# Kernel optimization log

Hardware: AMD Instinct MI355X
Metric: run time of the kernel (lower is better)

## Reference

```python
import jax, jax.numpy as jnp
import numpy as np

G = 500          # num graphs
NODES_PER_G = 1000
EDGES_PER_G = 2000
N = G * NODES_PER_G   # 500_000 total nodes
E = G * EDGES_PER_G   # 1_000_000 total edges
DN, DE, DG, DO = 128, 64, 128, 128


def setup_inputs() -> dict:
    key = jax.random.key(0)
    ks = jax.random.split(key, 7)
    return {
        "node_features": jax.random.normal(ks[0], (N, DN), dtype=jnp.float32),
        "edge_features": jax.random.normal(ks[1], (E, DE), dtype=jnp.float32),
        "global_features": jax.random.normal(ks[2], (G, DG), dtype=jnp.float32),
        "W_node": jax.random.normal(ks[3], (DO, DN), dtype=jnp.float32) / np.sqrt(DN),
        "W_edges": jax.random.normal(ks[4], (DO, DE), dtype=jnp.float32) / np.sqrt(DE),
        "W_global": jax.random.normal(ks[5], (DO, DG), dtype=jnp.float32) / np.sqrt(DG),
        "bias": jax.random.normal(ks[6], (DO,), dtype=jnp.float32) * 0.01,
        "num_nodes_by_graph": jnp.full((G,), NODES_PER_G, dtype=jnp.int32),
        "num_edges_by_graph": jnp.full((G,), EDGES_PER_G, dtype=jnp.int32),
    }


def _segment_mean(feats, lengths, num_segments, total):
    # segment ids from per-graph lengths (segment_lengths_to_ids)
    ids = jnp.repeat(jnp.arange(num_segments, dtype=jnp.int32), lengths,
                     total_repeat_length=total)
    s = jax.ops.segment_sum(feats, ids, num_segments=num_segments)
    cnt = jnp.maximum(lengths, 1).astype(feats.dtype)[:, None]
    return s / cnt


def reference(node_features, edge_features, global_features,
              W_node, W_edges, W_global, bias,
              num_nodes_by_graph, num_edges_by_graph):
    # mean-aggregate nodes/edges per graph, then linear projections summed
    node_agg = _segment_mean(node_features, num_nodes_by_graph, G, N)   # [G, DN]
    edge_agg = _segment_mean(edge_features, num_edges_by_graph, G, E)   # [G, DE]
    out = (jnp.einsum('gd,od->go', node_agg, W_node)
           + jnp.einsum('gd,od->go', edge_agg, W_edges)
           + jnp.einsum('gd,od->go', global_features, W_global)
           + bias)
    return out
```

## Files before the change

kernel.cpp:

```cpp
#include <hip/hip_runtime.h>


#define DN 128
#define DE 64
#define DO 128
#define NODE_SPLIT 4
#define EDGE_SPLIT 8

typedef float f4v __attribute__((ext_vector_type(4)));

__device__ __forceinline__ f4v nt_load(const f4v* p) {
    return __builtin_nontemporal_load(p);
}

__global__ __launch_bounds__(512) void scan_offsets_kernel(
    const int* __restrict__ nlen, const int* __restrict__ elen, int G,
    int* __restrict__ noff, int* __restrict__ eoff)
{
    __shared__ int sn[512], se[512];
    __shared__ int carry_n, carry_e;
    const int t = threadIdx.x;
    if (t == 0) { carry_n = 0; carry_e = 0; }
    __syncthreads();

    for (int base = 0; base < G; base += 512) {
        const int idx = base + t;
        const int vn = (idx < G) ? nlen[idx] : 0;
        const int ve = (idx < G) ? elen[idx] : 0;
        sn[t] = vn; se[t] = ve;
        __syncthreads();
        for (int off = 1; off < 512; off <<= 1) {
            const int an = (t >= off) ? sn[t - off] : 0;
            const int ae = (t >= off) ? se[t - off] : 0;
            __syncthreads();
            sn[t] += an; se[t] += ae;
            __syncthreads();
        }
        if (idx < G) {
            noff[idx] = carry_n + sn[t] - vn;
            eoff[idx] = carry_e + se[t] - ve;
        }
        __syncthreads();
        if (t == 0) {
            const int last = (G - base < 512) ? (G - base - 1) : 511;
            carry_n += sn[last];
            carry_e += se[last];
        }
        __syncthreads();
    }
}

__global__ __launch_bounds__(256) void agg_kernel(
    const float* __restrict__ nodes, const float* __restrict__ edges,
    const int* __restrict__ noff, const int* __restrict__ eoff,
    const int* __restrict__ nlen, const int* __restrict__ elen,
    float* __restrict__ nsum, float* __restrict__ esum, int G)
{
    __shared__ f4v sm[256];
    const int b = blockIdx.x;
    const int t = threadIdx.x;

    if (b < G * NODE_SPLIT) {
        const int g = b / NODE_SPLIT;
        const int c = b % NODE_SPLIT;
        const int len = nlen[g];
        const int off = noff[g];
        const int chunk = (len + NODE_SPLIT - 1) / NODE_SPLIT;
        const int r0 = c * chunk;
        const int r1 = (r0 + chunk < len) ? (r0 + chunk) : len;
        const int span = (r1 > r0) ? (r1 - r0) : 0;
        const int main_end = r0 + (span & ~31);

        const int col = t & 31;
        const int rl  = t >> 5;
        const f4v* __restrict__ base = (const f4v*)nodes;

        f4v a0 = {0.f,0.f,0.f,0.f}, a1 = a0, a2 = a0, a3 = a0;
        for (int rr = r0 + rl * 4; rr < main_end; rr += 32) {
            const size_t p = (size_t)(off + rr) * (DN / 4) + col;
            a0 += nt_load(base + p);
            a1 += nt_load(base + p + (DN / 4));
            a2 += nt_load(base + p + 2 * (DN / 4));
            a3 += nt_load(base + p + 3 * (DN / 4));
        }
        for (int r = main_end + rl; r < r1; r += 8) {
            a0 += nt_load(base + (size_t)(off + r) * (DN / 4) + col);
        }
        const f4v acc = (a0 + a1) + (a2 + a3);

        sm[t] = acc;
        __syncthreads();
        for (int s = 128; s >= 32; s >>= 1) {
            if (t < s) sm[t] += sm[t + s];
            __syncthreads();
        }
        if (t < 32) {
            const f4v v = sm[t];
            float* dst = &nsum[(size_t)g * DN + col * 4];
            atomicAdd(dst + 0, v.x);
            atomicAdd(dst + 1, v.y);
            atomicAdd(dst + 2, v.z);
            atomicAdd(dst + 3, v.w);
        }
    } else {
        const int bb = b - G * NODE_SPLIT;
        const int g = bb / EDGE_SPLIT;
        const int c = bb % EDGE_SPLIT;
        const int len = elen[g];
        const int off = eoff[g];
        const int chunk = (len + EDGE_SPLIT - 1) / EDGE_SPLIT;
        const int r0 = c * chunk;
        const int r1 = (r0 + chunk < len) ? (r0 + chunk) : len;
        const int span = (r1 > r0) ? (r1 - r0) : 0;
        const int main_end = r0 + (span & ~63);

        const int col = t & 15;
        const int rl  = t >> 4;
        const f4v* __restrict__ base = (const f4v*)edges;

        f4v a0 = {0.f,0.f,0.f,0.f}, a1 = a0, a2 = a0, a3 = a0;
        for (int rr = r0 + rl * 4; rr < main_end; rr += 64) {
            const size_t p = (size_t)(off + rr) * (DE / 4) + col;
            a0 += nt_load(base + p);
            a1 += nt_load(base + p + (DE / 4));
            a2 += nt_load(base + p + 2 * (DE / 4));
            a3 += nt_load(base + p + 3 * (DE / 4));
        }
        for (int r = main_end + rl; r < r1; r += 16) {
            a0 += nt_load(base + (size_t)(off + r) * (DE / 4) + col);
        }
        const f4v acc = (a0 + a1) + (a2 + a3);

        sm[t] = acc;
        __syncthreads();
        for (int s = 128; s >= 16; s >>= 1) {
            if (t < s) sm[t] += sm[t + s];
            __syncthreads();
        }
        if (t < 16) {
            const f4v v = sm[t];
            float* dst = &esum[(size_t)g * DE + col * 4];
            atomicAdd(dst + 0, v.x);
            atomicAdd(dst + 1, v.y);
            atomicAdd(dst + 2, v.z);
            atomicAdd(dst + 3, v.w);
        }
    }
}

__global__ __launch_bounds__(128) void finalize_kernel(
    const float* __restrict__ nsum, const float* __restrict__ esum,
    const float* __restrict__ glob,
    const float* __restrict__ Wn, const float* __restrict__ We,
    const float* __restrict__ Wg, const float* __restrict__ bias,
    const int* __restrict__ nlen, const int* __restrict__ elen,
    float* __restrict__ out)
{
    __shared__ float sn[DN], se_[DE], sg[DN];
    const int g = blockIdx.x;
    const int o = threadIdx.x;

    const int nl = nlen[g];
    const int el = elen[g];
    const float inv_n = 1.0f / (float)((nl > 1) ? nl : 1);
    const float inv_e = 1.0f / (float)((el > 1) ? el : 1);

    sn[o] = nsum[(size_t)g * DN + o] * inv_n;
    sg[o] = glob[(size_t)g * DN + o];
    if (o < DE) se_[o] = esum[(size_t)g * DE + o] * inv_e;
    __syncthreads();

    float acc = bias[o];
    const float4* __restrict__ wn = (const float4*)(Wn + (size_t)o * DN);
    const float4* __restrict__ wg = (const float4*)(Wg + (size_t)o * DN);
    const float4* __restrict__ we = (const float4*)(We + (size_t)o * DE);
    const float4* s4n = (const float4*)sn;
    const float4* s4g = (const float4*)sg;
    const float4* s4e = (const float4*)se_;

    #pragma unroll
    for (int i = 0; i < DN / 4; ++i) {
        const float4 a = wn[i], v = s4n[i];
        acc += a.x * v.x + a.y * v.y + a.z * v.z + a.w * v.w;
    }
    #pragma unroll
    for (int i = 0; i < DN / 4; ++i) {
        const float4 a = wg[i], v = s4g[i];
        acc += a.x * v.x + a.y * v.y + a.z * v.z + a.w * v.w;
    }
    #pragma unroll
    for (int i = 0; i < DE / 4; ++i) {
        const float4 a = we[i], v = s4e[i];
        acc += a.x * v.x + a.y * v.y + a.z * v.z + a.w * v.w;
    }
    out[(size_t)g * DO + o] = acc;
}

extern "C" void kernel_launch(void* const* d_in, const int* in_sizes, int n_in,
                              void* d_out, int out_size, void* d_ws, size_t ws_size,
                              hipStream_t stream)
{
    const float* nodes = (const float*)d_in[0];
    const float* edges = (const float*)d_in[1];
    const float* glob  = (const float*)d_in[2];
    const float* Wn    = (const float*)d_in[3];
    const float* We    = (const float*)d_in[4];
    const float* Wg    = (const float*)d_in[5];
    const float* bias  = (const float*)d_in[6];
    const int*   nlen  = (const int*)d_in[7];
    const int*   elen  = (const int*)d_in[8];
    float*       out   = (float*)d_out;

    const int G = in_sizes[7];

    float* nsum = (float*)d_ws;
    float* esum = nsum + (size_t)G * DN;
    int*   noff = (int*)(esum + (size_t)G * DE);
    int*   eoff = noff + G;

    hipMemsetAsync(d_ws, 0, (size_t)G * (DN + DE) * sizeof(float), stream);

    scan_offsets_kernel<<<1, 512, 0, stream>>>(nlen, elen, G, noff, eoff);

    const int agg_blocks = G * (NODE_SPLIT + EDGE_SPLIT);
    agg_kernel<<<agg_blocks, 256, 0, stream>>>(nodes, edges, noff, eoff,
                                               nlen, elen, nsum, esum, G);

    finalize_kernel<<<G, 128, 0, stream>>>(nsum, esum, glob, Wn, We, Wg, bias,
                                           nlen, elen, out);
}
```

Before: 481.2 us.

## Remove scan kernel and memset; compute offsets in-block and write partial sums

After: 475.1 us. No clear change (-1.3%).

```diff
diff --git a/kernel.cpp b/kernel.cpp
--- a/kernel.cpp
+++ b/kernel.cpp
@@ -5,7 +5,7 @@
 #define DE 64
 #define DO 128
 #define NODE_SPLIT 4
-#define EDGE_SPLIT 8
+#define EDGE_SPLIT 4
 
 typedef float f4v __attribute__((ext_vector_type(4)));
 
@@ -13,64 +13,41 @@
     return __builtin_nontemporal_load(p);
 }
 
-__global__ __launch_bounds__(512) void scan_offsets_kernel(
-    const int* __restrict__ nlen, const int* __restrict__ elen, int G,
-    int* __restrict__ noff, int* __restrict__ eoff)
-{
-    __shared__ int sn[512], se[512];
-    __shared__ int carry_n, carry_e;
-    const int t = threadIdx.x;
-    if (t == 0) { carry_n = 0; carry_e = 0; }
-    __syncthreads();
-
-    for (int base = 0; base < G; base += 512) {
-        const int idx = base + t;
-        const int vn = (idx < G) ? nlen[idx] : 0;
-        const int ve = (idx < G) ? elen[idx] : 0;
-        sn[t] = vn; se[t] = ve;
-        __syncthreads();
-        for (int off = 1; off < 512; off <<= 1) {
-            const int an = (t >= off) ? sn[t - off] : 0;
-            const int ae = (t >= off) ? se[t - off] : 0;
-            __syncthreads();
-            sn[t] += an; se[t] += ae;
-            __syncthreads();
-        }
-        if (idx < G) {
-            noff[idx] = carry_n + sn[t] - vn;
-            eoff[idx] = carry_e + se[t] - ve;
-        }
-        __syncthreads();
-        if (t == 0) {
-            const int last = (G - base < 512) ? (G - base - 1) : 511;
-            carry_n += sn[last];
-            carry_e += se[last];
-        }
-        __syncthreads();
-    }
-}
-
 __global__ __launch_bounds__(256) void agg_kernel(
     const float* __restrict__ nodes, const float* __restrict__ edges,
-    const int* __restrict__ noff, const int* __restrict__ eoff,
     const int* __restrict__ nlen, const int* __restrict__ elen,
     float* __restrict__ nsum, float* __restrict__ esum, int G)
 {
+    __shared__ int ired[256];
     __shared__ f4v sm[256];
     const int b = blockIdx.x;
     const int t = threadIdx.x;
 
-    if (b < G * NODE_SPLIT) {
-        const int g = b / NODE_SPLIT;
-        const int c = b % NODE_SPLIT;
-        const int len = nlen[g];
-        const int off = noff[g];
-        const int chunk = (len + NODE_SPLIT - 1) / NODE_SPLIT;
-        const int r0 = c * chunk;
-        const int r1 = (r0 + chunk < len) ? (r0 + chunk) : len;
-        const int span = (r1 > r0) ? (r1 - r0) : 0;
+    const bool is_node = (b < G * NODE_SPLIT);
+    const int gb = is_node ? b : (b - G * NODE_SPLIT);
+    const int g = gb / NODE_SPLIT;
+    const int c = gb % NODE_SPLIT;
+    const int* __restrict__ larr = is_node ? nlen : elen;
+
+    int part = 0;
+    for (int i = t; i < g; i += 256) part += larr[i];
+    ired[t] = part;
+    __syncthreads();
+    #pragma unroll
+    for (int s = 128; s >= 1; s >>= 1) {
+        if (t < s) ired[t] += ired[t + s];
+        __syncthreads();
+    }
+    const int off = ired[0];
+    const int len = larr[g];
+
+    const int chunk = (len + NODE_SPLIT - 1) / NODE_SPLIT;
+    const int r0 = (c * chunk < len) ? c * chunk : len;
+    const int r1 = (c * chunk + chunk < len) ? (c * chunk + chunk) : len;
+    const int span = r1 - r0;
+
+    if (is_node) {
         const int main_end = r0 + (span & ~31);
-
         const int col = t & 31;
         const int rl  = t >> 5;
         const f4v* __restrict__ base = (const f4v*)nodes;
@@ -86,34 +63,19 @@
         for (int r = main_end + rl; r < r1; r += 8) {
             a0 += nt_load(base + (size_t)(off + r) * (DN / 4) + col);
         }
-        const f4v acc = (a0 + a1) + (a2 + a3);
-
-        sm[t] = acc;
+        sm[t] = (a0 + a1) + (a2 + a3);
         __syncthreads();
+        #pragma unroll
         for (int s = 128; s >= 32; s >>= 1) {
             if (t < s) sm[t] += sm[t + s];
             __syncthreads();
         }
         if (t < 32) {
-            const f4v v = sm[t];
-            float* dst = &nsum[(size_t)g * DN + col * 4];
-            atomicAdd(dst + 0, v.x);
-            atomicAdd(dst + 1, v.y);
-            atomicAdd(dst + 2, v.z);
-            atomicAdd(dst + 3, v.w);
+            f4v* dst = (f4v*)&nsum[((size_t)g * NODE_SPLIT + c) * DN];
+            dst[t] = sm[t];
         }
     } else {
-        const int bb = b - G * NODE_SPLIT;
-        const int g = bb / EDGE_SPLIT;
-        const int c = bb % EDGE_SPLIT;
-        const int len = elen[g];
-        const int off = eoff[g];
-        const int chunk = (len + EDGE_SPLIT - 1) / EDGE_SPLIT;
-        const int r0 = c * chunk;
-        const int r1 = (r0 + chunk < len) ? (r0 + chunk) : len;
-        const int span = (r1 > r0) ? (r1 - r0) : 0;
         const int main_end = r0 + (span & ~63);
-
         const int col = t & 15;
         const int rl  = t >> 4;
         const f4v* __restrict__ base = (const f4v*)edges;
@@ -129,21 +91,16 @@
         for (int r = main_end + rl; r < r1; r += 16) {
             a0 += nt_load(base + (size_t)(off + r) * (DE / 4) + col);
         }
-        const f4v acc = (a0 + a1) + (a2 + a3);
-
-        sm[t] = acc;
+        sm[t] = (a0 + a1) + (a2 + a3);
         __syncthreads();
+        #pragma unroll
         for (int s = 128; s >= 16; s >>= 1) {
             if (t < s) sm[t] += sm[t + s];
             __syncthreads();
         }
         if (t < 16) {
-            const f4v v = sm[t];
-            float* dst = &esum[(size_t)g * DE + col * 4];
-            atomicAdd(dst + 0, v.x);
-            atomicAdd(dst + 1, v.y);
-            atomicAdd(dst + 2, v.z);
-            atomicAdd(dst + 3, v.w);
+            f4v* dst = (f4v*)&esum[((size_t)g * EDGE_SPLIT + c) * DE];
+            dst[t] = sm[t];
         }
     }
 }
@@ -165,9 +122,19 @@
     const float inv_n = 1.0f / (float)((nl > 1) ? nl : 1);
     const float inv_e = 1.0f / (float)((el > 1) ? el : 1);
 
-    sn[o] = nsum[(size_t)g * DN + o] * inv_n;
+    float accn = 0.f;
+    #pragma unroll
+    for (int s = 0; s < NODE_SPLIT; ++s)
+        accn += nsum[((size_t)g * NODE_SPLIT + s) * DN + o];
+    sn[o] = accn * inv_n;
     sg[o] = glob[(size_t)g * DN + o];
-    if (o < DE) se_[o] = esum[(size_t)g * DE + o] * inv_e;
+    if (o < DE) {
+        float acce = 0.f;
+        #pragma unroll
+        for (int s = 0; s < EDGE_SPLIT; ++s)
+            acce += esum[((size_t)g * EDGE_SPLIT + s) * DE + o];
+        se_[o] = acce * inv_e;
+    }
     __syncthreads();
 
     float acc = bias[o];
@@ -214,17 +181,11 @@
     const int G = in_sizes[7];
 
     float* nsum = (float*)d_ws;
-    float* esum = nsum + (size_t)G * DN;
-    int*   noff = (int*)(esum + (size_t)G * DE);
-    int*   eoff = noff + G;
-
-    hipMemsetAsync(d_ws, 0, (size_t)G * (DN + DE) * sizeof(float), stream);
-
-    scan_offsets_kernel<<<1, 512, 0, stream>>>(nlen, elen, G, noff, eoff);
+    float* esum = nsum + (size_t)G * NODE_SPLIT * DN;
 
     const int agg_blocks = G * (NODE_SPLIT + EDGE_SPLIT);
-    agg_kernel<<<agg_blocks, 256, 0, stream>>>(nodes, edges, noff, eoff,
-                                               nlen, elen, nsum, esum, G);
+    agg_kernel<<<agg_blocks, 256, 0, stream>>>(nodes, edges, nlen, elen,
+                                               nsum, esum, G);
 
     finalize_kernel<<<G, 128, 0, stream>>>(nsum, esum, glob, Wn, We, Wg, bias,
                                            nlen, elen, out);
```
